# Kernel optimization log

Measured on AMD Instinct MI355X. Metric: run time of the kernel, lower is better.

## Reference

```python
import jax, jax.numpy as jnp
import numpy as np

EPS = 1e-10
BETA = 0.25


def setup_inputs() -> dict:
    key = jax.random.key(0)
    k1, k2 = jax.random.split(key)
    z = jax.random.normal(k1, (32, 256, 32, 32), dtype=jnp.float32)
    # codebook initialized uniform(-1/K, 1/K) in the original; scale doesn't affect math shape
    K = 1024
    codebook = jax.random.uniform(k2, (K, 256), dtype=jnp.float32,
                                  minval=-1.0 / K, maxval=1.0 / K)
    return {"z": z, "codebook": codebook}


def reference(z, codebook):
    b, d, h, w = z.shape
    K = codebook.shape[0]
    # (b d h w) -> (b h w, d)
    z_flat = jnp.transpose(z, (0, 2, 3, 1)).reshape(-1, d)  # [N, d]
    N = z_flat.shape[0]

    # squared L2 distances: ||z||^2 + ||c||^2 - 2 z.c  -> [N, K]
    distances = (jnp.sum(z_flat ** 2, axis=1, keepdims=True)
                 + jnp.sum(codebook ** 2, axis=1)
                 - 2.0 * jnp.einsum('nd,kd->nk', z_flat, codebook))

    encoding_indices = jnp.argmin(distances, axis=1)  # [N]

    # codebook usage histogram == mean of one-hot encodings over N
    encodings_mean = jnp.zeros((K,), dtype=z.dtype).at[encoding_indices].add(1.0) / N
    perplexity = jnp.exp(-jnp.sum(encodings_mean * jnp.log(encodings_mean + EPS)))

    zq_flat = codebook[encoding_indices]  # [N, d]
    z_quantized = jnp.transpose(zq_flat.reshape(b, h, w, d), (0, 3, 1, 2))

    mse = jnp.mean((z_quantized - z) ** 2)
    loss = BETA * mse + mse  # encoder + codebook terms are numerically equal in fwd

    quantized_st = z + jax.lax.stop_gradient(z_quantized - z)
    return (quantized_st, loss, perplexity, encoding_indices, distances)
```

## Files before the change

kernel.cpp:

```cpp
#include <hip/hip_runtime.h>
#include <hip/hip_bf16.h>
#include <math.h>

constexpr int D = 256;
constexpr int N = 32768;
constexpr int K = 1024;
constexpr float MARGIN = 8e-4f;

constexpr int OFF_Q    = 0;
constexpr int OFF_LOSS = 8388608;
constexpr int OFF_PERP = 8388609;
constexpr int OFF_IDX  = 8388610;
constexpr int OFF_DIST = 8421378;

using f32x4 = __attribute__((ext_vector_type(4))) float;
using s16x8 = __attribute__((ext_vector_type(8))) short;
using u16x8 = __attribute__((ext_vector_type(8))) unsigned short;
using u16x4 = __attribute__((ext_vector_type(4))) unsigned short;

#define GLOAD_LDS16(g, l)                                                     \
    __builtin_amdgcn_global_load_lds(                                         \
        (const __attribute__((address_space(1))) void*)(g),                   \
        (__attribute__((address_space(3))) void*)(l), 16, 0, 0)

__device__ __forceinline__ unsigned short bf16_bits(float v) {
    __hip_bfloat16 h = __float2bfloat16(v);
    return *(unsigned short*)&h;
}

__global__ __launch_bounds__(256) void split_z_kernel(const float* __restrict__ z,
                                                      const float* __restrict__ cb,
                                                      unsigned short* __restrict__ A,
                                                      float* __restrict__ znorm,
                                                      unsigned short* __restrict__ Bb,
                                                      float* __restrict__ cnorm,
                                                      int* __restrict__ hist) {
    int t = threadIdx.x;
    if (blockIdx.y == 32) {
        int gid = blockIdx.x * 256 + t;
        if (gid < K) hist[gid] = 0;
        int lane = t & 63, wv = t >> 6;
        #pragma unroll 4
        for (int i = 0; i < 16; ++i) {
            int k = blockIdx.x * 64 + wv * 16 + i;
            float4 v = *(const float4*)(cb + (size_t)k * D + lane * 4);
            unsigned short hb[4] = {bf16_bits(v.x), bf16_bits(v.y),
                                    bf16_bits(v.z), bf16_bits(v.w)};
            *(u16x4*)(Bb + (size_t)k * D + lane * 4) = *(u16x4*)&hb[0];
            float s = v.x * v.x + v.y * v.y + v.z * v.z + v.w * v.w;
            #pragma unroll
            for (int off = 32; off; off >>= 1) s += __shfl_down(s, off, 64);
            if (lane == 0) cnorm[k] = s;
        }
        return;
    }

    __shared__ float tile[64][65];
    __shared__ float znp[64][4];
    int r0 = blockIdx.x * 64;
    int b  = blockIdx.y;
    const float* zb = z + (size_t)b * D * 1024;
    int rr4 = (t & 15) * 4;
    int rr = t >> 2, chunk = t & 3;
    size_t n = (size_t)b * 1024 + r0 + rr;
    float zacc = 0.f;

    for (int dblk = 0; dblk < 4; ++dblk) {
        int d0 = dblk * 64;
        if (dblk) __syncthreads();
        #pragma unroll
        for (int i = 0; i < 4; ++i) {
            int di = i * 16 + (t >> 4);
            float4 v = *(const float4*)(zb + (size_t)(d0 + di) * 1024 + r0 + rr4);
            *(float4*)&tile[di][rr4] = v;
        }
        __syncthreads();

        unsigned short hbuf[16];
        #pragma unroll
        for (int i = 0; i < 16; ++i) {
            float v = tile[chunk * 16 + i][rr];
            hbuf[i] = bf16_bits(v);
            zacc += v * v;
        }
        unsigned short* pa = A + n * 256 + d0 + chunk * 16;
        *(u16x8*)(pa + 0) = *(u16x8*)&hbuf[0];
        *(u16x8*)(pa + 8) = *(u16x8*)&hbuf[8];
    }
    znp[rr][chunk] = zacc;
    __syncthreads();
    if (t < 64) {
        float s = znp[t][0] + znp[t][1] + znp[t][2] + znp[t][3];
        znorm[(size_t)b * 1024 + r0 + t] = s;
    }
}

__global__ __launch_bounds__(256) void dist_gemm_mfma(const unsigned short* __restrict__ A,
                                                      const unsigned short* __restrict__ Bb,
                                                      const float* __restrict__ znorm,
                                                      const float* __restrict__ cnorm,
                                                      float* __restrict__ dist,
                                                      float* __restrict__ pmin,
                                                      unsigned long long* __restrict__ pmask) {
    __shared__ unsigned short As[128 * 64];
    __shared__ unsigned short Bs[128 * 64];

    int t = threadIdx.x;
    int l = t & 63;
    int w = t >> 6;
    int p = blockIdx.x;
    int xcd = p & 7, j = p >> 3;
    int nb = xcd * 32 + (j >> 3);
    int kbl = j & 7;
    int k0 = kbl * 128;
    int n0 = nb * 128;

    int srow = t >> 3;
    int scol = (t & 7) * 8;
    const unsigned short* Ab = A + ((size_t)(n0 + srow)) * 256 + scol;
    const unsigned short* Bbp = Bb + ((size_t)(k0 + srow)) * 256 + scol;
    unsigned short* AsBase = As + t * 8;
    unsigned short* BsBase = Bs + t * 8;

    f32x4 acc[4][4];
    #pragma unroll
    for (int i = 0; i < 4; ++i)
        #pragma unroll
        for (int jj = 0; jj < 4; ++jj) acc[i][jj] = (f32x4){0.f, 0.f, 0.f, 0.f};

    int wr = w >> 1, wc = w & 1;
    int aRowBase = wr * 64 + (l & 15);
    int bRowBase = wc * 64 + (l & 15);
    int kLane = (l >> 4) * 8;

    #pragma unroll
    for (int kt = 0; kt < 4; ++kt) {
        int col = kt * 64;
        #pragma unroll
        for (int pass = 0; pass < 4; ++pass) {
            GLOAD_LDS16(Ab + (size_t)pass * 32 * 256 + col, AsBase + pass * 2048);
            GLOAD_LDS16(Bbp + (size_t)pass * 32 * 256 + col, BsBase + pass * 2048);
        }
        __syncthreads();

        #pragma unroll
        for (int kk = 0; kk < 64; kk += 32) {
            s16x8 af[4], bf[4];
            #pragma unroll
            for (int mf = 0; mf < 4; ++mf)
                af[mf] = *(const s16x8*)&As[(aRowBase + mf * 16) * 64 + kk + kLane];
            #pragma unroll
            for (int nf = 0; nf < 4; ++nf)
                bf[nf] = *(const s16x8*)&Bs[(bRowBase + nf * 16) * 64 + kk + kLane];
            #pragma unroll
            for (int mf = 0; mf < 4; ++mf)
                #pragma unroll
                for (int nf = 0; nf < 4; ++nf)
                    acc[mf][nf] = __builtin_amdgcn_mfma_f32_16x16x32_bf16(
                        af[mf], bf[nf], acc[mf][nf], 0, 0, 0);
        }
        if (kt < 3) __syncthreads();
    }

    int colBase = k0 + wc * 64 + (l & 15);
    int rowBase = n0 + wr * 64 + (l >> 4) * 4;
    int kb = kbl * 2 + wc;
    int g = l >> 4;
    float cn[4];
    #pragma unroll
    for (int nf = 0; nf < 4; ++nf) cn[nf] = cnorm[colBase + nf * 16];
    #pragma unroll
    for (int mf = 0; mf < 4; ++mf) {
        #pragma unroll
        for (int r = 0; r < 4; ++r) {
            int n = rowBase + mf * 16 + r;
            float zn = znorm[n];
            float* pr = dist + (size_t)n * K;
            float dv[4];
            #pragma unroll
            for (int nf = 0; nf < 4; ++nf) {
                dv[nf] = zn + cn[nf] - 2.0f * acc[mf][nf][r];
                pr[colBase + nf * 16] = dv[nf];
            }
            float m4 = fminf(fminf(dv[0], dv[1]), fminf(dv[2], dv[3]));
            #pragma unroll
            for (int off = 1; off < 16; off <<= 1)
                m4 = fminf(m4, __shfl_xor(m4, off, 64));
            float th = m4 + MARGIN;
            unsigned long long bal[4];
            #pragma unroll
            for (int nf = 0; nf < 4; ++nf)
                bal[nf] = __ballot(dv[nf] <= th);
            if ((l & 15) == 0) {
                unsigned long long msk = 0;
                #pragma unroll
                for (int nf = 0; nf < 4; ++nf)
                    msk |= ((bal[nf] >> (g * 16)) & 0xFFFFULL) << (nf * 16);
                pmin[(size_t)n * 16 + kb] = m4;
                pmask[(size_t)n * 16 + kb] = msk;
            }
        }
    }
}

__global__ __launch_bounds__(256) void resolve_kernel(const float* __restrict__ pmin,
                                                      const unsigned long long* __restrict__ pmask,
                                                      const float* __restrict__ z,
                                                      const float* __restrict__ cb,
                                                      const float* __restrict__ znorm,
                                                      const float* __restrict__ cnorm,
                                                      int* __restrict__ idx_i,
                                                      float* __restrict__ out_idx,
                                                      int* __restrict__ hist,
                                                      float* __restrict__ mse_part) {
    __shared__ float s4[4];
    int n = blockIdx.x * 4 + (threadIdx.x >> 6);
    int lane = threadIdx.x & 63;
    int s16 = lane & 15;

    float myp = pmin[(size_t)n * 16 + s16];
    float gmin = myp;
    #pragma unroll
    for (int off = 1; off < 16; off <<= 1)
        gmin = fminf(gmin, __shfl_xor(gmin, off, 64));
    float th = gmin + MARGIN;

    unsigned long long mym = (myp <= th) ? pmask[(size_t)n * 16 + s16] : 0ULL;
    int total = __popcll(mym);
    #pragma unroll
    for (int off = 1; off < 16; off <<= 1)
        total += __shfl_xor(total, off, 64);

    int besti;
    if (total == 1) {
        int cand = mym ? (s16 * 64 + __builtin_ctzll(mym)) : 0x7fffffff;
        #pragma unroll
        for (int off = 1; off < 16; off <<= 1)
            cand = min(cand, __shfl_xor(cand, off, 64));
        besti = cand;
    } else {
        int b = n >> 10, r = n & 1023;
        const float* zb = z + (size_t)b * D * 1024 + r;
        float zv[4];
        #pragma unroll
        for (int q = 0; q < 4; ++q)
            zv[q] = zb[(size_t)(lane + 64 * q) * 1024];
        float zn = znorm[n];
        float bestv = INFINITY;
        besti = 0x7fffffff;
        for (int kb = 0; kb < 16; ++kb) {
            unsigned long long m = __shfl(mym, kb, 64);
            while (m) {
                int lb = __builtin_ctzll(m);
                m &= m - 1;
                int k = kb * 64 + lb;
                const float* cr = cb + (size_t)k * D + lane;
                float s = zv[0] * cr[0] + zv[1] * cr[64] + zv[2] * cr[128] + zv[3] * cr[192];
                #pragma unroll
                for (int off = 1; off < 64; off <<= 1)
                    s += __shfl_xor(s, off, 64);
                float dd = zn + cnorm[k] - 2.0f * s;
                if (dd < bestv) { bestv = dd; besti = k; }
            }
        }
    }

    if (lane == 0) {
        idx_i[n] = besti;
        out_idx[n] = (float)besti;
        atomicAdd(&hist[besti], 1);
        s4[threadIdx.x >> 6] = gmin;
    }
    __syncthreads();
    if (threadIdx.x == 0)
        mse_part[blockIdx.x] = (s4[0] + s4[1]) + (s4[2] + s4[3]);
}

__global__ __launch_bounds__(256) void gather_kernel(const float* __restrict__ cb,
                                                     const int* __restrict__ idx_i,
                                                     float* __restrict__ out_q,
                                                     const float* __restrict__ mse_part,
                                                     const int* __restrict__ hist,
                                                     float* __restrict__ out) {
    int t = threadIdx.x;
    int n = blockIdx.x * 256 + t;
    int b = n >> 10, r = n & 1023;
    float* qp = out_q + (size_t)b * D * 1024 + r;
    const float* crow = cb + (size_t)idx_i[n] * D;
    int c0 = blockIdx.y * 32;

    #pragma unroll
    for (int c = 0; c < 32; c += 4) {
        float4 v = *(const float4*)(crow + c0 + c);
        qp[(size_t)(c0 + c + 0) * 1024] = v.x;
        qp[(size_t)(c0 + c + 1) * 1024] = v.y;
        qp[(size_t)(c0 + c + 2) * 1024] = v.z;
        qp[(size_t)(c0 + c + 3) * 1024] = v.w;
    }

    if (blockIdx.x == 0 && blockIdx.y == 0) {
        __shared__ float red[256];
        float s = 0.f;
        for (int i = t; i < 8192; i += 256) s += mse_part[i];
        red[t] = s;
        __syncthreads();
        #pragma unroll
        for (int off = 128; off; off >>= 1) {
            if (t < off) red[t] += red[t + off];
            __syncthreads();
        }
        float msesum = red[0];
        __syncthreads();
        float e = 0.f;
        for (int k = t; k < K; k += 256) {
            float p = (float)hist[k] * (1.0f / (float)N);
            e += p * logf(p + 1e-10f);
        }
        red[t] = e;
        __syncthreads();
        #pragma unroll
        for (int off = 128; off; off >>= 1) {
            if (t < off) red[t] += red[t + off];
            __syncthreads();
        }
        if (t == 0) {
            float mse = msesum / (float)((size_t)N * D);
            out[OFF_LOSS] = 1.25f * mse;
            out[OFF_PERP] = expf(-red[0]);
        }
    }
}

extern "C" void kernel_launch(void* const* d_in, const int* in_sizes, int n_in,
                              void* d_out, int out_size, void* d_ws, size_t ws_size,
                              hipStream_t stream) {
    const float* z  = (const float*)d_in[0];
    const float* cb = (const float*)d_in[1];
    float* out = (float*)d_out;

    char* wsb = (char*)d_ws;
    size_t off = 0;
    unsigned short* A  = (unsigned short*)(wsb + off); off += (size_t)N * 256 * 2;
    unsigned short* Bb = (unsigned short*)(wsb + off); off += (size_t)K * 256 * 2;
    float* pmin        = (float*)(wsb + off);          off += (size_t)N * 16 * 4;
    unsigned long long* pmask = (unsigned long long*)(wsb + off); off += (size_t)N * 16 * 8;
    float* znorm       = (float*)(wsb + off);          off += (size_t)N * 4;
    float* cnorm       = (float*)(wsb + off);          off += (size_t)K * 4;
    float* mse_part    = (float*)(wsb + off);          off += 8192 * 4;
    int* hist          = (int*)(wsb + off);            off += (size_t)K * 4;
    int* idx_i         = (int*)(wsb + off);

    split_z_kernel<<<dim3(16, 33), 256, 0, stream>>>(z, cb, A, znorm, Bb, cnorm, hist);
    dist_gemm_mfma<<<2048, 256, 0, stream>>>(A, Bb, znorm, cnorm,
                                             out + OFF_DIST, pmin, pmask);
    resolve_kernel<<<N / 4, 256, 0, stream>>>(pmin, pmask, z, cb, znorm, cnorm,
                                              idx_i, out + OFF_IDX, hist, mse_part);
    gather_kernel<<<dim3(128, 8), 256, 0, stream>>>(cb, idx_i, out + OFF_Q,
                                                    mse_part, hist, out);
}
```

Measured before the change: 108.9 us.

## Fuse z transpose and bf16 conversion into distance GEMM A-tile load

Removes the separate split_z pass that wrote a bf16 transposed copy of z to workspace. The GEMM now loads fp32 z tiles straight into LDS, converts them to bf16 into a swizzled A tile, and computes the row norms in the same pass, using them from LDS in the epilogue. This saves the round trip through the intermediate A buffer and one kernel launch. The cost is that each z tile is reloaded and converted by all 8 codebook-column blocks, and each K step gains extra syncs and LDS traffic.

```diff
diff --git a/kernel.cpp b/kernel.cpp
--- a/kernel.cpp
+++ b/kernel.cpp
@@ -28,80 +28,36 @@
     return *(unsigned short*)&h;
 }
 
-__global__ __launch_bounds__(256) void split_z_kernel(const float* __restrict__ z,
-                                                      const float* __restrict__ cb,
-                                                      unsigned short* __restrict__ A,
-                                                      float* __restrict__ znorm,
-                                                      unsigned short* __restrict__ Bb,
-                                                      float* __restrict__ cnorm,
-                                                      int* __restrict__ hist) {
+__global__ __launch_bounds__(256) void cb_prep(const float* __restrict__ cb,
+                                               unsigned short* __restrict__ Bb,
+                                               float* __restrict__ cnorm,
+                                               int* __restrict__ hist) {
     int t = threadIdx.x;
-    if (blockIdx.y == 32) {
-        int gid = blockIdx.x * 256 + t;
-        if (gid < K) hist[gid] = 0;
-        int lane = t & 63, wv = t >> 6;
-        #pragma unroll 4
-        for (int i = 0; i < 16; ++i) {
-            int k = blockIdx.x * 64 + wv * 16 + i;
-            float4 v = *(const float4*)(cb + (size_t)k * D + lane * 4);
-            unsigned short hb[4] = {bf16_bits(v.x), bf16_bits(v.y),
-                                    bf16_bits(v.z), bf16_bits(v.w)};
-            *(u16x4*)(Bb + (size_t)k * D + lane * 4) = *(u16x4*)&hb[0];
-            float s = v.x * v.x + v.y * v.y + v.z * v.z + v.w * v.w;
-            #pragma unroll
-            for (int off = 32; off; off >>= 1) s += __shfl_down(s, off, 64);
-            if (lane == 0) cnorm[k] = s;
-        }
-        return;
-    }
-
-    __shared__ float tile[64][65];
-    __shared__ float znp[64][4];
-    int r0 = blockIdx.x * 64;
-    int b  = blockIdx.y;
-    const float* zb = z + (size_t)b * D * 1024;
-    int rr4 = (t & 15) * 4;
-    int rr = t >> 2, chunk = t & 3;
-    size_t n = (size_t)b * 1024 + r0 + rr;
-    float zacc = 0.f;
-
-    for (int dblk = 0; dblk < 4; ++dblk) {
-        int d0 = dblk * 64;
-        if (dblk) __syncthreads();
-        #pragma unroll
-        for (int i = 0; i < 4; ++i) {
-            int di = i * 16 + (t >> 4);
-            float4 v = *(const float4*)(zb + (size_t)(d0 + di) * 1024 + r0 + rr4);
-            *(float4*)&tile[di][rr4] = v;
-        }
-        __syncthreads();
-
-        unsigned short hbuf[16];
-        #pragma unroll
-        for (int i = 0; i < 16; ++i) {
-            float v = tile[chunk * 16 + i][rr];
-            hbuf[i] = bf16_bits(v);
-            zacc += v * v;
-        }
-        unsigned short* pa = A + n * 256 + d0 + chunk * 16;
-        *(u16x8*)(pa + 0) = *(u16x8*)&hbuf[0];
-        *(u16x8*)(pa + 8) = *(u16x8*)&hbuf[8];
-    }
-    znp[rr][chunk] = zacc;
-    __syncthreads();
-    if (t < 64) {
-        float s = znp[t][0] + znp[t][1] + znp[t][2] + znp[t][3];
-        znorm[(size_t)b * 1024 + r0 + t] = s;
-    }
-}
-
-__global__ __launch_bounds__(256) void dist_gemm_mfma(const unsigned short* __restrict__ A,
-                                                      const unsigned short* __restrict__ Bb,
-                                                      const float* __restrict__ znorm,
-                                                      const float* __restrict__ cnorm,
-                                                      float* __restrict__ dist,
-                                                      float* __restrict__ pmin,
-                                                      unsigned long long* __restrict__ pmask) {
+    int gid = blockIdx.x * 256 + t;
+    if (gid < K) hist[gid] = 0;
+    int lane = t & 63, wv = t >> 6;
+    #pragma unroll 4
+    for (int i = 0; i < 16; ++i) {
+        int k = blockIdx.x * 64 + wv * 16 + i;
+        float4 v = *(const float4*)(cb + (size_t)k * D + lane * 4);
+        unsigned short hb[4] = {bf16_bits(v.x), bf16_bits(v.y),
+                                bf16_bits(v.z), bf16_bits(v.w)};
+        *(u16x4*)(Bb + (size_t)k * D + lane * 4) = *(u16x4*)&hb[0];
+        float s = v.x * v.x + v.y * v.y + v.z * v.z + v.w * v.w;
+        #pragma unroll
+        for (int off = 32; off; off >>= 1) s += __shfl_down(s, off, 64);
+        if (lane == 0) cnorm[k] = s;
+    }
+}
+
+__global__ __launch_bounds__(256) void dist_gemm_fused(const float* __restrict__ z,
+                                                       const unsigned short* __restrict__ Bb,
+                                                       const float* __restrict__ cnorm,
+                                                       float* __restrict__ dist,
+                                                       float* __restrict__ pmin,
+                                                       unsigned long long* __restrict__ pmask,
+                                                       float* __restrict__ znorm) {
+    __shared__ float Zf[64 * 64];
     __shared__ unsigned short As[128 * 64];
     __shared__ unsigned short Bs[128 * 64];
 
@@ -114,41 +70,71 @@
     int kbl = j & 7;
     int k0 = kbl * 128;
     int n0 = nb * 128;
-
-    int srow = t >> 3;
-    int scol = (t & 7) * 8;
-    const unsigned short* Ab = A + ((size_t)(n0 + srow)) * 256 + scol;
+    int b = nb >> 3;
+    int r0 = (nb & 7) * 128;
+
+    int srow = t >> 3, scol = (t & 7) * 8;
     const unsigned short* Bbp = Bb + ((size_t)(k0 + srow)) * 256 + scol;
-    unsigned short* AsBase = As + t * 8;
     unsigned short* BsBase = Bs + t * 8;
+    float* ZfBase = Zf + t * 4;
+
+    int rp = t & 31;
+    int dgr = t >> 5;
 
     f32x4 acc[4][4];
     #pragma unroll
     for (int i = 0; i < 4; ++i)
         #pragma unroll
         for (int jj = 0; jj < 4; ++jj) acc[i][jj] = (f32x4){0.f, 0.f, 0.f, 0.f};
+
+    float za00 = 0.f, za01 = 0.f, za10 = 0.f, za11 = 0.f;
 
     int wr = w >> 1, wc = w & 1;
     int aRowBase = wr * 64 + (l & 15);
     int bRowBase = wc * 64 + (l & 15);
     int kLane = (l >> 4) * 8;
-
-    #pragma unroll
+    int rdSwA = (l & 7) * 8;
+
     for (int kt = 0; kt < 4; ++kt) {
-        int col = kt * 64;
-        #pragma unroll
-        for (int pass = 0; pass < 4; ++pass) {
-            GLOAD_LDS16(Ab + (size_t)pass * 32 * 256 + col, AsBase + pass * 2048);
-            GLOAD_LDS16(Bbp + (size_t)pass * 32 * 256 + col, BsBase + pass * 2048);
-        }
-        __syncthreads();
+        int d0 = kt * 64;
+        #pragma unroll
+        for (int pass = 0; pass < 4; ++pass)
+            GLOAD_LDS16(Bbp + (size_t)pass * 32 * 256 + d0, BsBase + pass * 2048);
+
+        #pragma unroll
+        for (int h = 0; h < 2; ++h) {
+            const float* zsrc = z + ((size_t)(b * 256 + d0 + (t >> 4))) * 1024
+                                  + r0 + h * 64 + (t & 15) * 4;
+            #pragma unroll
+            for (int pass = 0; pass < 4; ++pass)
+                GLOAD_LDS16(zsrc + (size_t)pass * 16 * 1024, ZfBase + pass * 1024);
+            __syncthreads();
+
+            float2 v[8];
+            #pragma unroll
+            for (int i = 0; i < 8; ++i)
+                v[i] = *(const float2*)&Zf[(dgr * 8 + i) * 64 + 2 * rp];
+            unsigned short h0[8], h1[8];
+            float s0 = 0.f, s1 = 0.f;
+            #pragma unroll
+            for (int i = 0; i < 8; ++i) {
+                h0[i] = bf16_bits(v[i].x); s0 += v[i].x * v[i].x;
+                h1[i] = bf16_bits(v[i].y); s1 += v[i].y * v[i].y;
+            }
+            if (h == 0) { za00 += s0; za01 += s1; } else { za10 += s0; za11 += s1; }
+            int row0 = h * 64 + 2 * rp;
+            int row1 = row0 + 1;
+            *(u16x8*)&As[row0 * 64 + ((dgr * 8) ^ ((row0 & 7) << 3))] = *(u16x8*)&h0[0];
+            *(u16x8*)&As[row1 * 64 + ((dgr * 8) ^ ((row1 & 7) << 3))] = *(u16x8*)&h1[0];
+            __syncthreads();
+        }
 
         #pragma unroll
         for (int kk = 0; kk < 64; kk += 32) {
             s16x8 af[4], bf[4];
             #pragma unroll
             for (int mf = 0; mf < 4; ++mf)
-                af[mf] = *(const s16x8*)&As[(aRowBase + mf * 16) * 64 + kk + kLane];
+                af[mf] = *(const s16x8*)&As[(aRowBase + mf * 16) * 64 + ((kk + kLane) ^ rdSwA)];
             #pragma unroll
             for (int nf = 0; nf < 4; ++nf)
                 bf[nf] = *(const s16x8*)&Bs[(bRowBase + nf * 16) * 64 + kk + kLane];
@@ -159,11 +145,27 @@
                     acc[mf][nf] = __builtin_amdgcn_mfma_f32_16x16x32_bf16(
                         af[mf], bf[nf], acc[mf][nf], 0, 0, 0);
         }
-        if (kt < 3) __syncthreads();
-    }
+        __syncthreads();
+    }
+
+    float* znp = Zf;
+    float* znsum = Zf + 1024;
+    znp[(2 * rp) * 8 + dgr]          = za00;
+    znp[(2 * rp + 1) * 8 + dgr]      = za01;
+    znp[(64 + 2 * rp) * 8 + dgr]     = za10;
+    znp[(64 + 2 * rp + 1) * 8 + dgr] = za11;
+    __syncthreads();
+    if (t < 128) {
+        float s = 0.f;
+        #pragma unroll
+        for (int g = 0; g < 8; ++g) s += znp[t * 8 + g];
+        znsum[t] = s;
+    }
+    __syncthreads();
+    if (kbl == 0 && t < 128) znorm[n0 + t] = znsum[t];
 
     int colBase = k0 + wc * 64 + (l & 15);
-    int rowBase = n0 + wr * 64 + (l >> 4) * 4;
+    int lrowBase = wr * 64 + (l >> 4) * 4;
     int kb = kbl * 2 + wc;
     int g = l >> 4;
     float cn[4];
@@ -173,8 +175,9 @@
     for (int mf = 0; mf < 4; ++mf) {
         #pragma unroll
         for (int r = 0; r < 4; ++r) {
-            int n = rowBase + mf * 16 + r;
-            float zn = znorm[n];
+            int lrow = lrowBase + mf * 16 + r;
+            int n = n0 + lrow;
+            float zn = znsum[lrow];
             float* pr = dist + (size_t)n * K;
             float dv[4];
             #pragma unroll
@@ -340,7 +343,6 @@
 
     char* wsb = (char*)d_ws;
     size_t off = 0;
-    unsigned short* A  = (unsigned short*)(wsb + off); off += (size_t)N * 256 * 2;
     unsigned short* Bb = (unsigned short*)(wsb + off); off += (size_t)K * 256 * 2;
     float* pmin        = (float*)(wsb + off);          off += (size_t)N * 16 * 4;
     unsigned long long* pmask = (unsigned long long*)(wsb + off); off += (size_t)N * 16 * 8;
@@ -350,9 +352,9 @@
     int* hist          = (int*)(wsb + off);            off += (size_t)K * 4;
     int* idx_i         = (int*)(wsb + off);
 
-    split_z_kernel<<<dim3(16, 33), 256, 0, stream>>>(z, cb, A, znorm, Bb, cnorm, hist);
-    dist_gemm_mfma<<<2048, 256, 0, stream>>>(A, Bb, znorm, cnorm,
-                                             out + OFF_DIST, pmin, pmask);
+    cb_prep<<<16, 256, 0, stream>>>(cb, Bb, cnorm, hist);
+    dist_gemm_fused<<<2048, 256, 0, stream>>>(z, Bb, cnorm,
+                                              out + OFF_DIST, pmin, pmask, znorm);
     resolve_kernel<<<N / 4, 256, 0, stream>>>(pmin, pmask, z, cb, znorm, cnorm,
                                               idx_i, out + OFF_IDX, hist, mse_part);
     gather_kernel<<<dim3(128, 8), 256, 0, stream>>>(cb, idx_i, out + OFF_Q,
```

Result: slower. 121.2 us (+11.4%).
